# Optimization experiments

Measured on AMD Instinct MI355X. Metric: run time of the kernel, lower is better.

## Reference

```python
import jax, jax.numpy as jnp
import numpy as np

B, S, D, H, E, K = 4, 2048, 1024, 4096, 8, 2
CAP_RATIO = 1.05


def setup_inputs() -> dict:
    key = jax.random.key(0)
    k0, k1, k2, k3 = jax.random.split(key, 4)
    x = jax.random.normal(k0, (B, S, D), jnp.float32)
    # router gating weight (xavier-uniform-ish scale)
    Wg = jax.random.normal(k1, (E, D), jnp.float32) * np.float32(np.sqrt(2.0 / (D + E)))
    W1 = jax.random.normal(k2, (E, D, H), jnp.float32) * np.float32(0.02)
    b1 = jnp.zeros((E, H), jnp.float32)
    W2 = jax.random.normal(k3, (E, H, D), jnp.float32) * np.float32(0.02)
    b2 = jnp.zeros((E, D), jnp.float32)
    return {"x": x, "Wg": Wg, "W1": W1, "b1": b1, "W2": W2, "b2": b2}


def reference(x, Wg, W1, b1, W2, b2):
    Bs, Ss, Dd = x.shape
    T = Bs * Ss
    C = int(round(K * T * CAP_RATIO / E))  # static buffer capacity per expert
    xf = x.reshape(T, Dd)

    # --- router (eval mode: no noise) ---
    logits = xf @ Wg.T                       # (T, E)
    gates = jax.nn.softmax(logits, axis=-1)  # (T, E)
    topv, topi = jax.lax.top_k(gates, K)     # (T, K)

    # --- capacity-limited dispatch: FCFS over slot-major (slot, token) order ---
    idx_sm = topi.T.reshape(-1)                              # (K*T,) slot-major expert ids
    oh = jax.nn.one_hot(idx_sm, E, dtype=jnp.int32)          # (K*T, E)
    pos_sm = (jnp.cumsum(oh, axis=0) * oh).sum(-1) - 1       # 0-based rank within expert
    within_sm = pos_sm < C
    pos_sm = jnp.where(within_sm, pos_sm, C)                 # C == out-of-bounds sentinel
    pos = pos_sm.reshape(K, T).T                             # (T, K)
    within = within_sm.reshape(K, T).T                       # (T, K) bool

    # --- combine weights: mask dropped slots, renormalize over active slots ---
    w = topv * within.astype(topv.dtype)
    sums = w.sum(-1, keepdims=True)
    w = jnp.where(sums > 0, w / sums, w)

    # --- scatter tokens into per-expert capacity buffers ---
    e_flat = topi.reshape(-1)                                # (T*K,)
    pos_flat = pos.reshape(-1)                               # (T*K,)
    x_ts = jnp.broadcast_to(xf[:, None, :], (T, K, Dd)).reshape(T * K, Dd)
    expert_in = jnp.zeros((E, C, Dd), x.dtype).at[e_flat, pos_flat].set(x_ts, mode='drop')

    # --- per-expert MLP (grouped GEMM) ---
    h = jax.nn.gelu(jnp.einsum('ecd,edh->ech', expert_in, W1) + b1[:, None, :], approximate=False)
    o = jnp.einsum('ech,ehd->ecd', h, W2) + b2[:, None, :]   # (E, C, D)

    # --- gather back and weighted combine (dropped slots gather 0) ---
    y_ts = o.at[e_flat, pos_flat].get(mode='fill', fill_value=0).reshape(T, K, Dd)
    y = jnp.einsum('tk,tkd->td', w, y_ts)                    # (T, D)

    # --- auxiliary losses ---
    imp = gates.sum(0)                                       # (E,)
    l_imp = (jnp.std(imp) / (imp.mean() + 1e-6)) ** 2
    tpe = (oh * within_sm[:, None].astype(jnp.int32)).sum(0).astype(jnp.float32)
    l_load = (jnp.std(tpe) / (tpe.mean() + 1e-6)) ** 2
    l_aux = 0.5 * (l_imp + l_load)

    return y.reshape(Bs, Ss, Dd), l_aux, l_load
```

## Files before the change

kernel.cpp:

```cpp
#include <hip/hip_runtime.h>
#include <math.h>

typedef short short8v __attribute__((ext_vector_type(8)));
typedef float f32x4 __attribute__((ext_vector_type(4)));
typedef unsigned short ushort4v __attribute__((ext_vector_type(4)));

#define T_TOK 8192
#define DDIM 1024
#define HDIM 4096
#define NE 8
#define CCAP 2150
#define CPAD 2304

__device__ __forceinline__ unsigned short f2bf(float f) {
  union { float f; unsigned u; } a; a.f = f;
  unsigned r = a.u + 0x7fffu + ((a.u >> 16) & 1u);
  return (unsigned short)(r >> 16);
}
__device__ __forceinline__ float bf2f(unsigned short h) {
  union { unsigned u; float f; } a; a.u = ((unsigned)h) << 16;
  return a.f;
}

__global__ __launch_bounds__(256) void router_kernel(
    const float* __restrict__ x, const float* __restrict__ Wg,
    int2* __restrict__ topi, float2* __restrict__ topv,
    float* __restrict__ blkimp) {
  __shared__ float wg[NE * DDIM];
  __shared__ float gsh[4][NE];
  int tid = threadIdx.x;
  for (int i = tid; i < NE * DDIM / 4; i += 256)
    ((float4*)wg)[i] = ((const float4*)Wg)[i];
  __syncthreads();
  int w = tid >> 6, lane = tid & 63;
  int t = blockIdx.x * 4 + w;
  const float* xr = x + (size_t)t * DDIM;
  float p[NE] = {0.f, 0.f, 0.f, 0.f, 0.f, 0.f, 0.f, 0.f};
#pragma unroll
  for (int j = 0; j < 16; ++j) {
    float xv = xr[lane + 64 * j];
#pragma unroll
    for (int e = 0; e < NE; ++e)
      p[e] = fmaf(xv, wg[e * DDIM + lane + 64 * j], p[e]);
  }
#pragma unroll
  for (int e = 0; e < NE; ++e) {
#pragma unroll
    for (int off = 32; off > 0; off >>= 1) p[e] += __shfl_xor(p[e], off, 64);
  }
  float mx = p[0];
#pragma unroll
  for (int e = 1; e < NE; ++e) mx = fmaxf(mx, p[e]);
  float g[NE];
  float s = 0.f;
#pragma unroll
  for (int e = 0; e < NE; ++e) { g[e] = expf(p[e] - mx); s += g[e]; }
  float inv = 1.0f / s;
#pragma unroll
  for (int e = 0; e < NE; ++e) g[e] *= inv;
  int i0 = 0; float v0 = g[0];
#pragma unroll
  for (int e = 1; e < NE; ++e) if (g[e] > v0) { v0 = g[e]; i0 = e; }
  int i1 = -1; float v1 = -1.0f;
#pragma unroll
  for (int e = 0; e < NE; ++e)
    if (e != i0 && g[e] > v1) { v1 = g[e]; i1 = e; }
  if (lane == 0) {
    topi[t] = make_int2(i0, i1);
    topv[t] = make_float2(v0, v1);
#pragma unroll
    for (int e = 0; e < NE; ++e) gsh[w][e] = g[e];
  }
  __syncthreads();
  if (tid < NE)
    blkimp[blockIdx.x * NE + tid] =
        gsh[0][tid] + gsh[1][tid] + gsh[2][tid] + gsh[3][tid];
}

__global__ __launch_bounds__(256) void dispatch_kernel(
    const int2* __restrict__ topi, const float2* __restrict__ topv,
    const float* __restrict__ blkimp, int2* __restrict__ posmj,
    float2* __restrict__ wmaj, float* __restrict__ tail) {
  __shared__ unsigned char eid[2 * T_TOK];
  __shared__ unsigned short possm[2 * T_TOK];
  __shared__ int cnt_sh[NE];
  __shared__ float part[32][NE];
  int tid = threadIdx.x;
  for (int i = tid; i < T_TOK; i += 256) {
    int2 ti = topi[i];
    eid[i] = (unsigned char)ti.x;
    eid[T_TOK + i] = (unsigned char)ti.y;
  }
  __syncthreads();
  if (tid < 64) {
    int lane = tid;
    unsigned long long low = (1ull << lane) - 1ull;
    int c0 = 0, c1 = 0, c2 = 0, c3 = 0, c4 = 0, c5 = 0, c6 = 0, c7 = 0;
    for (int base = 0; base < 2 * T_TOK; base += 64) {
      int e = eid[base + lane];
      unsigned long long m0 = __ballot(e == 0);
      unsigned long long m1 = __ballot(e == 1);
      unsigned long long m2 = __ballot(e == 2);
      unsigned long long m3 = __ballot(e == 3);
      unsigned long long m4 = __ballot(e == 4);
      unsigned long long m5 = __ballot(e == 5);
      unsigned long long m6 = __ballot(e == 6);
      unsigned long long m7 = __ballot(e == 7);
      int rank = 0;
      if (e == 0) rank = c0 + __popcll(m0 & low);
      if (e == 1) rank = c1 + __popcll(m1 & low);
      if (e == 2) rank = c2 + __popcll(m2 & low);
      if (e == 3) rank = c3 + __popcll(m3 & low);
      if (e == 4) rank = c4 + __popcll(m4 & low);
      if (e == 5) rank = c5 + __popcll(m5 & low);
      if (e == 6) rank = c6 + __popcll(m6 & low);
      if (e == 7) rank = c7 + __popcll(m7 & low);
      possm[base + lane] = (unsigned short)((rank < CCAP) ? rank : CCAP);
      c0 += __popcll(m0); c1 += __popcll(m1); c2 += __popcll(m2);
      c3 += __popcll(m3); c4 += __popcll(m4); c5 += __popcll(m5);
      c6 += __popcll(m6); c7 += __popcll(m7);
    }
    if (lane == 0) {
      cnt_sh[0] = c0; cnt_sh[1] = c1; cnt_sh[2] = c2; cnt_sh[3] = c3;
      cnt_sh[4] = c4; cnt_sh[5] = c5; cnt_sh[6] = c6; cnt_sh[7] = c7;
    }
  }
  __syncthreads();
  for (int t = tid; t < T_TOK; t += 256) {
    int p0 = possm[t], p1 = possm[T_TOK + t];
    float2 tv = topv[t];
    float w0 = (p0 < CCAP) ? tv.x : 0.0f;
    float w1 = (p1 < CCAP) ? tv.y : 0.0f;
    float s = w0 + w1;
    if (s > 0.0f) { w0 /= s; w1 /= s; }
    posmj[t] = make_int2(p0, p1);
    wmaj[t] = make_float2(w0, w1);
  }
  {
    int sl = tid >> 3, e8 = tid & 7;
    float s = 0.f;
    for (int b = sl; b < 2048; b += 32) s += blkimp[b * NE + e8];
    part[sl][e8] = s;
  }
  __syncthreads();
  if (tid == 0) {
    float imp[NE], te[NE];
    for (int e = 0; e < NE; ++e) {
      float s = 0.f;
      for (int j = 0; j < 32; ++j) s += part[j][e];
      imp[e] = s;
      int c = cnt_sh[e];
      te[e] = (float)(c < CCAP ? c : CCAP);
    }
    float mi = 0.f, mt = 0.f;
    for (int e = 0; e < NE; ++e) { mi += imp[e]; mt += te[e]; }
    mi *= 0.125f; mt *= 0.125f;
    float vi = 0.f, vt = 0.f;
    for (int e = 0; e < NE; ++e) {
      vi += (imp[e] - mi) * (imp[e] - mi);
      vt += (te[e] - mt) * (te[e] - mt);
    }
    vi *= 0.125f; vt *= 0.125f;
    float ai = sqrtf(vi) / (mi + 1e-6f);
    float at = sqrtf(vt) / (mt + 1e-6f);
    tail[0] = 0.5f * (ai * ai + at * at);
    tail[1] = at * at;
  }
}

__global__ __launch_bounds__(256) void scatter_kernel(
    const float* __restrict__ x, const int2* __restrict__ topi,
    const int2* __restrict__ posmj, unsigned short* __restrict__ ein) {
  int tid = threadIdx.x;
  int gid = blockIdx.x * 4 + (tid >> 6);
  int lane = tid & 63;
  int t = gid >> 1, k = gid & 1;
  int2 pp = posmj[t];
  int p = k ? pp.y : pp.x;
  if (p >= CCAP) return;
  int2 ii = topi[t];
  int e = k ? ii.y : ii.x;
  const float4* src = (const float4*)(x + (size_t)t * DDIM);
  unsigned short* dst = ein + ((size_t)e * CPAD + p) * DDIM;
#pragma unroll
  for (int j = 0; j < 4; ++j) {
    int c = j * 64 + lane;
    float4 v = src[c];
    ushort4v o;
    o.x = f2bf(v.x); o.y = f2bf(v.y); o.z = f2bf(v.z); o.w = f2bf(v.w);
    *(ushort4v*)(dst + (size_t)c * 4) = o;
  }
}

__global__ __launch_bounds__(256) void transpose_cvt_kernel(
    const float* __restrict__ W, unsigned short* __restrict__ WT, int R,
    int Cc) {
  __shared__ unsigned short tile[64][72];
  int rt = R >> 6, ct = Cc >> 6;
  int per_e = rt * ct;
  int e = blockIdx.x / per_e;
  int rem = blockIdx.x % per_e;
  int tr = rem % rt, tc = rem / rt;
  int r0 = tr << 6, c0 = tc << 6;
  const float* We = W + (size_t)e * R * Cc;
  unsigned short* WTe = WT + (size_t)e * R * Cc;
  int tid = threadIdx.x;
  {
    int rl = tid >> 2, cb = (tid & 3) << 4;
    const float* src = We + (size_t)(r0 + rl) * Cc + c0 + cb;
#pragma unroll
    for (int j = 0; j < 16; j += 4) {
      float4 v = *(const float4*)(src + j);
      tile[rl][cb + j + 0] = f2bf(v.x);
      tile[rl][cb + j + 1] = f2bf(v.y);
      tile[rl][cb + j + 2] = f2bf(v.z);
      tile[rl][cb + j + 3] = f2bf(v.w);
    }
  }
  __syncthreads();
  {
    int cl = tid >> 2, rb = (tid & 3) << 4;
    unsigned short* dst = WTe + (size_t)(c0 + cl) * R + r0 + rb;
#pragma unroll
    for (int j = 0; j < 16; j += 4) {
      ushort4v o;
      o.x = tile[rb + j + 0][cl];
      o.y = tile[rb + j + 1][cl];
      o.z = tile[rb + j + 2][cl];
      o.w = tile[rb + j + 3][cl];
      *(ushort4v*)(dst + j) = o;
    }
  }
}

template <bool GELU>
__global__ __launch_bounds__(512, 2) void gemm256_rs(
    const unsigned short* __restrict__ A, const unsigned short* __restrict__ B,
    const float* __restrict__ bias, unsigned short* __restrict__ Out0,
    unsigned short* __restrict__ Out1, int M, int N, int Kz, int Ksub, int NT,
    int mt, int nt) {
  __shared__ __align__(16) char smem[131072];
  int nwg = gridDim.x;
  int bid = blockIdx.x;
  int swz = (bid & 7) * (nwg >> 3) + (bid >> 3);
  int bm = swz % mt;
  int r = swz / mt;
  int bn = r % nt;
  int r2 = r / nt;
  int e = r2 & 7;
  int ks = r2 >> 3;
  unsigned short* Outp = ks ? Out1 : Out0;
  int koff = ks * Ksub;

  int tid = threadIdx.x;
  int w = tid >> 6, lane = tid & 63;
  int wm = w >> 2, wn = w & 3;
  int fr = lane & 15, g = lane >> 4;
  size_t Kzs = (size_t)Kz;
  const char* Ab = (const char*)(A + ((size_t)e * M + (size_t)bm * 256) * Kzs + koff);
  const char* Bb = (const char*)(B + ((size_t)e * N + (size_t)bn * 256) * Kzs + koff);

  size_t ro0 = (size_t)(w * 16 + fr) * Kzs * 2 + (size_t)g * 16;
  size_t ro1 = ro0 + (size_t)128 * Kzs * 2;
  int ld0 = (w << 10) + lane * 16;
  int ld1 = ((8 + w) << 10) + lane * 16;

  short8v st[8];
  auto gload = [&](const char* a, const char* b) {
    st[0] = *(const short8v*)(a + ro0);
    st[1] = *(const short8v*)(a + ro1);
    st[2] = *(const short8v*)(a + ro0 + 64);
    st[3] = *(const short8v*)(a + ro1 + 64);
    st[4] = *(const short8v*)(b + ro0);
    st[5] = *(const short8v*)(b + ro1);
    st[6] = *(const short8v*)(b + ro0 + 64);
    st[7] = *(const short8v*)(b + ro1 + 64);
  };
  auto swrite = [&](int buf) {
    char* p = smem + (buf << 15);
    *(short8v*)(p + ld0) = st[0];
    *(short8v*)(p + ld1) = st[1];
    *(short8v*)(p + 16384 + ld0) = st[2];
    *(short8v*)(p + 16384 + ld1) = st[3];
    *(short8v*)(p + 65536 + ld0) = st[4];
    *(short8v*)(p + 65536 + ld1) = st[5];
    *(short8v*)(p + 65536 + 16384 + ld0) = st[6];
    *(short8v*)(p + 65536 + 16384 + ld1) = st[7];
  };
  auto lda = [&](int buf, int kk, int m16) -> short8v {
    return *(const short8v*)(smem + (buf << 15) + (kk << 14) + (m16 << 10) +
                             lane * 16);
  };
  auto ldb = [&](int buf, int kk, int n16) -> short8v {
    return *(const short8v*)(smem + 65536 + (buf << 15) + (kk << 14) +
                             (n16 << 10) + lane * 16);
  };

  f32x4 acc[8][4] = {};

  gload(Ab, Bb);
  swrite(0);
  gload(Ab + 128, Bb + 128);
  __syncthreads();

  for (int t = 0; t < NT; ++t) {
    int c = t & 1;
#pragma unroll
    for (int kk = 0; kk < 2; ++kk) {
      short8v bv4[4], av;
#pragma unroll
      for (int n = 0; n < 4; ++n) bv4[n] = ldb(c, kk, wn * 4 + n);
#pragma unroll
      for (int m = 0; m < 8; ++m) {
        av = lda(c, kk, wm * 8 + m);
#pragma unroll
        for (int n = 0; n < 4; ++n)
          acc[m][n] = __builtin_amdgcn_mfma_f32_16x16x32_bf16(av, bv4[n],
                                                              acc[m][n], 0, 0, 0);
      }
    }
    if (t + 1 < NT) swrite(c ^ 1);
    if (t + 2 < NT)
      gload(Ab + (size_t)(t + 2) * 128, Bb + (size_t)(t + 2) * 128);
    __syncthreads();
  }

  float bv[4];
#pragma unroll
  for (int n = 0; n < 4; ++n)
    bv[n] = (ks == 0)
                ? bias[(size_t)e * N + (size_t)bn * 256 + wn * 64 + n * 16 + fr]
                : 0.0f;
  char* wreg = smem + w * 16384;
#pragma unroll
  for (int m = 0; m < 8; ++m)
#pragma unroll
    for (int n = 0; n < 4; ++n)
#pragma unroll
      for (int j = 0; j < 4; ++j) {
        float v = acc[m][n][j] + bv[n];
        if (GELU) v = 0.5f * v * (1.0f + erff(v * 0.70710678118654752f));
        int rl = m * 16 + g * 4 + j;
        *(unsigned short*)(wreg + rl * 128 + (n * 16 + fr) * 2) = f2bf(v);
      }
  unsigned short* Oe = Outp +
                       ((size_t)e * M + (size_t)bm * 256 + (size_t)wm * 128) * N +
                       (size_t)bn * 256 + (size_t)wn * 64;
#pragma unroll
  for (int pass = 0; pass < 16; ++pass) {
    int rr = pass * 8 + (lane >> 3);
    int ch = lane & 7;
    short8v vv = *(const short8v*)(wreg + rr * 128 + ch * 16);
    *(short8v*)(Oe + (size_t)rr * N + ch * 8) = vv;
  }
}

__global__ __launch_bounds__(256) void gather_kernel(
    const unsigned short* __restrict__ obufA,
    const unsigned short* __restrict__ obufB, const int2* __restrict__ topi,
    const int2* __restrict__ posmj, const float2* __restrict__ wmaj,
    float* __restrict__ y) {
  int tid = threadIdx.x;
  int w = tid >> 6, lane = tid & 63;
  int t = blockIdx.x * 4 + w;
  int2 pp = posmj[t];
  int2 ii = topi[t];
  float2 ww = wmaj[t];
  float* yr = y + (size_t)t * DDIM;
  size_t o0 = ((size_t)ii.x * CPAD + pp.x) * DDIM;
  size_t o1 = ((size_t)ii.y * CPAD + pp.y) * DDIM;
  bool v0 = pp.x < CCAP, v1 = pp.y < CCAP;
#pragma unroll
  for (int j = 0; j < 4; ++j) {
    int c = j * 64 + lane;
    float ax = 0.f, ay = 0.f, az = 0.f, aw = 0.f;
    if (v0) {
      ushort4v a = *(const ushort4v*)(obufA + o0 + (size_t)c * 4);
      ushort4v b = *(const ushort4v*)(obufB + o0 + (size_t)c * 4);
      ax += ww.x * (bf2f(a.x) + bf2f(b.x));
      ay += ww.x * (bf2f(a.y) + bf2f(b.y));
      az += ww.x * (bf2f(a.z) + bf2f(b.z));
      aw += ww.x * (bf2f(a.w) + bf2f(b.w));
    }
    if (v1) {
      ushort4v a = *(const ushort4v*)(obufA + o1 + (size_t)c * 4);
      ushort4v b = *(const ushort4v*)(obufB + o1 + (size_t)c * 4);
      ax += ww.y * (bf2f(a.x) + bf2f(b.x));
      ay += ww.y * (bf2f(a.y) + bf2f(b.y));
      az += ww.y * (bf2f(a.z) + bf2f(b.z));
      aw += ww.y * (bf2f(a.w) + bf2f(b.w));
    }
    ((float4*)yr)[c] = make_float4(ax, ay, az, aw);
  }
}

extern "C" void kernel_launch(void* const* d_in, const int* in_sizes, int n_in,
                              void* d_out, int out_size, void* d_ws,
                              size_t ws_size, hipStream_t stream) {
  (void)in_sizes; (void)n_in; (void)out_size; (void)ws_size;
  const float* x = (const float*)d_in[0];
  const float* Wg = (const float*)d_in[1];
  const float* W1 = (const float*)d_in[2];
  const float* b1 = (const float*)d_in[3];
  const float* W2 = (const float*)d_in[4];
  const float* b2 = (const float*)d_in[5];
  float* out = (float*)d_out;

  char* ws = (char*)d_ws;
  size_t off = 0;
  auto alloc = [&](size_t b) {
    char* p = ws + off;
    off += (b + 255) & ~(size_t)255;
    return p;
  };
  unsigned short* ein = (unsigned short*)alloc((size_t)NE * CPAD * DDIM * 2);
  unsigned short* hbuf = (unsigned short*)alloc((size_t)NE * CPAD * HDIM * 2);
  unsigned short* obuf = (unsigned short*)alloc((size_t)NE * CPAD * DDIM * 2);
  unsigned short* w1t = (unsigned short*)alloc((size_t)NE * HDIM * DDIM * 2);
  unsigned short* w2t = (unsigned short*)alloc((size_t)NE * DDIM * HDIM * 2);
  int2* topi = (int2*)alloc(T_TOK * sizeof(int2));
  float2* topv = (float2*)alloc(T_TOK * sizeof(float2));
  int2* posmj = (int2*)alloc(T_TOK * sizeof(int2));
  float2* wmaj = (float2*)alloc(T_TOK * sizeof(float2));
  float* blkimp = (float*)alloc(2048 * NE * sizeof(float));

  transpose_cvt_kernel<<<NE * (DDIM / 64) * (HDIM / 64), 256, 0, stream>>>(
      W1, w1t, DDIM, HDIM);
  transpose_cvt_kernel<<<NE * (HDIM / 64) * (DDIM / 64), 256, 0, stream>>>(
      W2, w2t, HDIM, DDIM);
  router_kernel<<<T_TOK / 4, 256, 0, stream>>>(x, Wg, topi, topv, blkimp);
  dispatch_kernel<<<1, 256, 0, stream>>>(topi, topv, blkimp, posmj, wmaj,
                                         out + (size_t)T_TOK * DDIM);
  scatter_kernel<<<(2 * T_TOK) / 4, 256, 0, stream>>>(x, topi, posmj, ein);

  gemm256_rs<true><<<NE * 9 * 16, 512, 0, stream>>>(
      ein, w1t, b1, hbuf, hbuf, CPAD, HDIM, DDIM, DDIM, DDIM / 64, 9, 16);
  gemm256_rs<false><<<NE * 9 * 4 * 2, 512, 0, stream>>>(
      hbuf, w2t, b2, obuf, ein, CPAD, DDIM, HDIM, HDIM / 2, HDIM / 128, 9, 4);

  gather_kernel<<<T_TOK / 4, 256, 0, stream>>>(obuf, ein, topi, posmj, wmaj,
                                               out);
}
```

Baseline: 665.8 us.

## Load GEMM operands directly from global memory into MFMA registers, dropping LDS staging

The grouped expert GEMMs no longer stage A/B tiles through double-buffered shared memory with barriers. Each wave now loads its MFMA operand fragments straight from global memory, and the K loop count becomes a template parameter so it can be unrolled. The epilogue is also reworked to write out through a small 4KB-per-wave buffer in four chunks, which cuts LDS to 32KB. This removes LDS traffic and block-wide syncs, but each fragment is re-read by several waves through L1/L2. The global loads are strided narrow row reads rather than coalesced tiles, and there is no software prefetch.

```diff
diff --git a/kernel.cpp b/kernel.cpp
--- a/kernel.cpp
+++ b/kernel.cpp
@@ -233,13 +233,13 @@
   }
 }
 
-template <bool GELU>
-__global__ __launch_bounds__(512, 2) void gemm256_rs(
+template <int NT, bool GELU>
+__global__ __launch_bounds__(512) void gemm256_nolds(
     const unsigned short* __restrict__ A, const unsigned short* __restrict__ B,
     const float* __restrict__ bias, unsigned short* __restrict__ Out0,
-    unsigned short* __restrict__ Out1, int M, int N, int Kz, int Ksub, int NT,
-    int mt, int nt) {
-  __shared__ __align__(16) char smem[131072];
+    unsigned short* __restrict__ Out1, int M, int N, int Kz, int Ksub, int mt,
+    int nt) {
+  __shared__ __align__(16) char smem[32768];
   int nwg = gridDim.x;
   int bid = blockIdx.x;
   int swz = (bid & 7) * (nwg >> 3) + (bid >> 3);
@@ -257,72 +257,33 @@
   int wm = w >> 2, wn = w & 3;
   int fr = lane & 15, g = lane >> 4;
   size_t Kzs = (size_t)Kz;
-  const char* Ab = (const char*)(A + ((size_t)e * M + (size_t)bm * 256) * Kzs + koff);
-  const char* Bb = (const char*)(B + ((size_t)e * N + (size_t)bn * 256) * Kzs + koff);
-
-  size_t ro0 = (size_t)(w * 16 + fr) * Kzs * 2 + (size_t)g * 16;
-  size_t ro1 = ro0 + (size_t)128 * Kzs * 2;
-  int ld0 = (w << 10) + lane * 16;
-  int ld1 = ((8 + w) << 10) + lane * 16;
-
-  short8v st[8];
-  auto gload = [&](const char* a, const char* b) {
-    st[0] = *(const short8v*)(a + ro0);
-    st[1] = *(const short8v*)(a + ro1);
-    st[2] = *(const short8v*)(a + ro0 + 64);
-    st[3] = *(const short8v*)(a + ro1 + 64);
-    st[4] = *(const short8v*)(b + ro0);
-    st[5] = *(const short8v*)(b + ro1);
-    st[6] = *(const short8v*)(b + ro0 + 64);
-    st[7] = *(const short8v*)(b + ro1 + 64);
-  };
-  auto swrite = [&](int buf) {
-    char* p = smem + (buf << 15);
-    *(short8v*)(p + ld0) = st[0];
-    *(short8v*)(p + ld1) = st[1];
-    *(short8v*)(p + 16384 + ld0) = st[2];
-    *(short8v*)(p + 16384 + ld1) = st[3];
-    *(short8v*)(p + 65536 + ld0) = st[4];
-    *(short8v*)(p + 65536 + ld1) = st[5];
-    *(short8v*)(p + 65536 + 16384 + ld0) = st[6];
-    *(short8v*)(p + 65536 + 16384 + ld1) = st[7];
-  };
-  auto lda = [&](int buf, int kk, int m16) -> short8v {
-    return *(const short8v*)(smem + (buf << 15) + (kk << 14) + (m16 << 10) +
-                             lane * 16);
-  };
-  auto ldb = [&](int buf, int kk, int n16) -> short8v {
-    return *(const short8v*)(smem + 65536 + (buf << 15) + (kk << 14) +
-                             (n16 << 10) + lane * 16);
-  };
+  const unsigned short* Ap =
+      A + ((size_t)e * M + (size_t)bm * 256 + wm * 128 + fr) * Kzs + koff +
+      g * 8;
+  const unsigned short* Bp =
+      B + ((size_t)e * N + (size_t)bn * 256 + wn * 64 + fr) * Kzs + koff +
+      g * 8;
 
   f32x4 acc[8][4] = {};
 
-  gload(Ab, Bb);
-  swrite(0);
-  gload(Ab + 128, Bb + 128);
-  __syncthreads();
-
+#pragma unroll 4
   for (int t = 0; t < NT; ++t) {
-    int c = t & 1;
 #pragma unroll
     for (int kk = 0; kk < 2; ++kk) {
-      short8v bv4[4], av;
-#pragma unroll
-      for (int n = 0; n < 4; ++n) bv4[n] = ldb(c, kk, wn * 4 + n);
+      int ko = t * 64 + kk * 32;
+      short8v Bv[4];
+#pragma unroll
+      for (int n = 0; n < 4; ++n)
+        Bv[n] = *(const short8v*)(Bp + (size_t)(n * 16) * Kzs + ko);
 #pragma unroll
       for (int m = 0; m < 8; ++m) {
-        av = lda(c, kk, wm * 8 + m);
+        short8v av = *(const short8v*)(Ap + (size_t)(m * 16) * Kzs + ko);
 #pragma unroll
         for (int n = 0; n < 4; ++n)
-          acc[m][n] = __builtin_amdgcn_mfma_f32_16x16x32_bf16(av, bv4[n],
+          acc[m][n] = __builtin_amdgcn_mfma_f32_16x16x32_bf16(av, Bv[n],
                                                               acc[m][n], 0, 0, 0);
       }
     }
-    if (t + 1 < NT) swrite(c ^ 1);
-    if (t + 2 < NT)
-      gload(Ab + (size_t)(t + 2) * 128, Bb + (size_t)(t + 2) * 128);
-    __syncthreads();
   }
 
   float bv[4];
@@ -331,27 +292,29 @@
     bv[n] = (ks == 0)
                 ? bias[(size_t)e * N + (size_t)bn * 256 + wn * 64 + n * 16 + fr]
                 : 0.0f;
-  char* wreg = smem + w * 16384;
-#pragma unroll
-  for (int m = 0; m < 8; ++m)
-#pragma unroll
-    for (int n = 0; n < 4; ++n)
-#pragma unroll
-      for (int j = 0; j < 4; ++j) {
-        float v = acc[m][n][j] + bv[n];
-        if (GELU) v = 0.5f * v * (1.0f + erff(v * 0.70710678118654752f));
-        int rl = m * 16 + g * 4 + j;
-        *(unsigned short*)(wreg + rl * 128 + (n * 16 + fr) * 2) = f2bf(v);
-      }
+  unsigned short* wb = (unsigned short*)(smem + w * 4096);
   unsigned short* Oe = Outp +
                        ((size_t)e * M + (size_t)bm * 256 + (size_t)wm * 128) * N +
                        (size_t)bn * 256 + (size_t)wn * 64;
 #pragma unroll
-  for (int pass = 0; pass < 16; ++pass) {
-    int rr = pass * 8 + (lane >> 3);
-    int ch = lane & 7;
-    short8v vv = *(const short8v*)(wreg + rr * 128 + ch * 16);
-    *(short8v*)(Oe + (size_t)rr * N + ch * 8) = vv;
+  for (int h = 0; h < 4; ++h) {
+#pragma unroll
+    for (int m2 = 0; m2 < 2; ++m2)
+#pragma unroll
+      for (int n = 0; n < 4; ++n)
+#pragma unroll
+        for (int j = 0; j < 4; ++j) {
+          float v = acc[h * 2 + m2][n][j] + bv[n];
+          if (GELU) v = 0.5f * v * (1.0f + erff(v * 0.70710678118654752f));
+          wb[(m2 * 16 + g * 4 + j) * 64 + n * 16 + fr] = f2bf(v);
+        }
+#pragma unroll
+    for (int p = 0; p < 4; ++p) {
+      int rr = p * 8 + (lane >> 3);
+      int ch = lane & 7;
+      short8v vv = *(const short8v*)(wb + rr * 64 + ch * 8);
+      *(short8v*)(Oe + (size_t)(h * 32 + rr) * N + ch * 8) = vv;
+    }
   }
 }
 
@@ -433,10 +396,10 @@
                                          out + (size_t)T_TOK * DDIM);
   scatter_kernel<<<(2 * T_TOK) / 4, 256, 0, stream>>>(x, topi, posmj, ein);
 
-  gemm256_rs<true><<<NE * 9 * 16, 512, 0, stream>>>(
-      ein, w1t, b1, hbuf, hbuf, CPAD, HDIM, DDIM, DDIM, DDIM / 64, 9, 16);
-  gemm256_rs<false><<<NE * 9 * 4 * 2, 512, 0, stream>>>(
-      hbuf, w2t, b2, obuf, ein, CPAD, DDIM, HDIM, HDIM / 2, HDIM / 128, 9, 4);
+  gemm256_nolds<16, true><<<NE * 9 * 16, 512, 0, stream>>>(
+      ein, w1t, b1, hbuf, hbuf, CPAD, HDIM, DDIM, DDIM, 9, 16);
+  gemm256_nolds<32, false><<<NE * 9 * 4 * 2, 512, 0, stream>>>(
+      hbuf, w2t, b2, obuf, ein, CPAD, DDIM, HDIM, HDIM / 2, 9, 4);
 
   gather_kernel<<<T_TOK / 4, 256, 0, stream>>>(obuf, ein, topi, posmj, wmaj,
                                                out);
```

Result: slower. 1.240 ms (+86.3%).

## Split first expert GEMM into 256-tile and 128-tile kernels to balance waves

Applied to the files above, without the earlier changes.

The first grouped GEMM (up-projection with GELU) is split by output column range. The first half of the N tiles stays on the 256x256 kernel, and the second half runs on a new 128x128-tile kernel with 256 threads. A bn0 offset parameter is added so each launch covers its own column range. The aim is to reduce wave quantization and tail imbalance across CUs. In exchange, the smaller tiles have lower arithmetic intensity and the change adds an extra launch.

```diff
diff --git a/kernel.cpp b/kernel.cpp
--- a/kernel.cpp
+++ b/kernel.cpp
@@ -238,14 +238,14 @@
     const unsigned short* __restrict__ A, const unsigned short* __restrict__ B,
     const float* __restrict__ bias, unsigned short* __restrict__ Out0,
     unsigned short* __restrict__ Out1, int M, int N, int Kz, int Ksub, int NT,
-    int mt, int nt) {
+    int mt, int nt, int bn0) {
   __shared__ __align__(16) char smem[131072];
   int nwg = gridDim.x;
   int bid = blockIdx.x;
   int swz = (bid & 7) * (nwg >> 3) + (bid >> 3);
   int bm = swz % mt;
   int r = swz / mt;
-  int bn = r % nt;
+  int bn = r % nt + bn0;
   int r2 = r / nt;
   int e = r2 & 7;
   int ks = r2 >> 3;
@@ -351,6 +351,120 @@
     int rr = pass * 8 + (lane >> 3);
     int ch = lane & 7;
     short8v vv = *(const short8v*)(wreg + rr * 128 + ch * 16);
+    *(short8v*)(Oe + (size_t)rr * N + ch * 8) = vv;
+  }
+}
+
+template <bool GELU>
+__global__ __launch_bounds__(256) void gemm128_rs(
+    const unsigned short* __restrict__ A, const unsigned short* __restrict__ B,
+    const float* __restrict__ bias, unsigned short* __restrict__ Out, int M,
+    int N, int Kz, int NT, int mt, int nt, int bn0) {
+  __shared__ __align__(16) char smem[65536];
+  int nwg = gridDim.x;
+  int bid = blockIdx.x;
+  int swz = (bid & 7) * (nwg >> 3) + (bid >> 3);
+  int bm = swz % mt;
+  int r = swz / mt;
+  int bn = r % nt + bn0;
+  int e = (r / nt) & 7;
+
+  int tid = threadIdx.x;
+  int w = tid >> 6, lane = tid & 63;
+  int wm = w >> 1, wn = w & 1;
+  int fr = lane & 15, g = lane >> 4;
+  size_t Kzs = (size_t)Kz;
+  const char* Ab = (const char*)(A + ((size_t)e * M + (size_t)bm * 128) * Kzs);
+  const char* Bb = (const char*)(B + ((size_t)e * N + (size_t)bn * 128) * Kzs);
+
+  size_t ro0 = (size_t)(w * 16 + fr) * Kzs * 2 + (size_t)g * 16;
+  size_t ro1 = ro0 + (size_t)64 * Kzs * 2;
+  int ld0 = (w << 10) + lane * 16;
+  int ld1 = ((4 + w) << 10) + lane * 16;
+
+  short8v st[8];
+  auto gload = [&](const char* a, const char* b) {
+    st[0] = *(const short8v*)(a + ro0);
+    st[1] = *(const short8v*)(a + ro1);
+    st[2] = *(const short8v*)(a + ro0 + 64);
+    st[3] = *(const short8v*)(a + ro1 + 64);
+    st[4] = *(const short8v*)(b + ro0);
+    st[5] = *(const short8v*)(b + ro1);
+    st[6] = *(const short8v*)(b + ro0 + 64);
+    st[7] = *(const short8v*)(b + ro1 + 64);
+  };
+  auto swrite = [&](int buf) {
+    char* p = smem + (buf << 14);
+    *(short8v*)(p + ld0) = st[0];
+    *(short8v*)(p + ld1) = st[1];
+    *(short8v*)(p + 8192 + ld0) = st[2];
+    *(short8v*)(p + 8192 + ld1) = st[3];
+    *(short8v*)(p + 32768 + ld0) = st[4];
+    *(short8v*)(p + 32768 + ld1) = st[5];
+    *(short8v*)(p + 32768 + 8192 + ld0) = st[6];
+    *(short8v*)(p + 32768 + 8192 + ld1) = st[7];
+  };
+  auto lda = [&](int buf, int kk, int m16) -> short8v {
+    return *(const short8v*)(smem + (buf << 14) + (kk << 13) + (m16 << 10) +
+                             lane * 16);
+  };
+  auto ldb = [&](int buf, int kk, int n16) -> short8v {
+    return *(const short8v*)(smem + 32768 + (buf << 14) + (kk << 13) +
+                             (n16 << 10) + lane * 16);
+  };
+
+  f32x4 acc[4][4] = {};
+
+  gload(Ab, Bb);
+  swrite(0);
+  gload(Ab + 128, Bb + 128);
+  __syncthreads();
+
+  for (int t = 0; t < NT; ++t) {
+    int c = t & 1;
+#pragma unroll
+    for (int kk = 0; kk < 2; ++kk) {
+      short8v bv4[4], av;
+#pragma unroll
+      for (int n = 0; n < 4; ++n) bv4[n] = ldb(c, kk, wn * 4 + n);
+#pragma unroll
+      for (int m = 0; m < 4; ++m) {
+        av = lda(c, kk, wm * 4 + m);
+#pragma unroll
+        for (int n = 0; n < 4; ++n)
+          acc[m][n] = __builtin_amdgcn_mfma_f32_16x16x32_bf16(av, bv4[n],
+                                                              acc[m][n], 0, 0, 0);
+      }
+    }
+    if (t + 1 < NT) swrite(c ^ 1);
+    if (t + 2 < NT)
+      gload(Ab + (size_t)(t + 2) * 128, Bb + (size_t)(t + 2) * 128);
+    __syncthreads();
+  }
+
+  float bv[4];
+#pragma unroll
+  for (int n = 0; n < 4; ++n)
+    bv[n] = bias[(size_t)e * N + (size_t)bn * 128 + wn * 64 + n * 16 + fr];
+  unsigned short* wb = (unsigned short*)(smem + w * 8192);
+#pragma unroll
+  for (int m = 0; m < 4; ++m)
+#pragma unroll
+    for (int n = 0; n < 4; ++n)
+#pragma unroll
+      for (int j = 0; j < 4; ++j) {
+        float v = acc[m][n][j] + bv[n];
+        if (GELU) v = 0.5f * v * (1.0f + erff(v * 0.70710678118654752f));
+        wb[(m * 16 + g * 4 + j) * 64 + n * 16 + fr] = f2bf(v);
+      }
+  unsigned short* Oe = Out + ((size_t)e * M + (size_t)bm * 128 +
+                              (size_t)wm * 64) * (size_t)N +
+                       (size_t)bn * 128 + (size_t)wn * 64;
+#pragma unroll
+  for (int p = 0; p < 8; ++p) {
+    int rr = p * 8 + (lane >> 3);
+    int ch = lane & 7;
+    short8v vv = *(const short8v*)(wb + rr * 64 + ch * 8);
     *(short8v*)(Oe + (size_t)rr * N + ch * 8) = vv;
   }
 }
@@ -433,10 +547,13 @@
                                          out + (size_t)T_TOK * DDIM);
   scatter_kernel<<<(2 * T_TOK) / 4, 256, 0, stream>>>(x, topi, posmj, ein);
 
-  gemm256_rs<true><<<NE * 9 * 16, 512, 0, stream>>>(
-      ein, w1t, b1, hbuf, hbuf, CPAD, HDIM, DDIM, DDIM, DDIM / 64, 9, 16);
+  gemm256_rs<true><<<NE * 9 * 8, 512, 0, stream>>>(
+      ein, w1t, b1, hbuf, hbuf, CPAD, HDIM, DDIM, DDIM, DDIM / 64, 9, 8, 0);
+  gemm128_rs<true><<<NE * 18 * 16, 256, 0, stream>>>(
+      ein, w1t, b1, hbuf, CPAD, HDIM, DDIM, DDIM / 64, 18, 16, 16);
   gemm256_rs<false><<<NE * 9 * 4 * 2, 512, 0, stream>>>(
-      hbuf, w2t, b2, obuf, ein, CPAD, DDIM, HDIM, HDIM / 2, HDIM / 128, 9, 4);
+      hbuf, w2t, b2, obuf, ein, CPAD, DDIM, HDIM, HDIM / 2, HDIM / 128, 9, 4,
+      0);
 
   gather_kernel<<<T_TOK / 4, 256, 0, stream>>>(obuf, ein, topi, posmj, wmaj,
                                                out);
```

New measurement: 747.2 us. 1.12x slower.

## Parallelize dispatch rank scan across four waves with chunked prefix sums

Applied to the files above, without the earlier changes.

The capacity ranking in the dispatch kernel previously ran serially on one wavefront over all 16384 slot entries. It now splits the work into 64 chunks of 256 entries. All four waves count per-expert occurrences in their chunks, one wave builds an exclusive prefix over the chunk counts with shuffles, and all four waves then assign ranks in parallel. This shortens the serial dependency chain in a single-block kernel, at the cost of a second pass over the expert ids and two extra barriers.

```diff
diff --git a/kernel.cpp b/kernel.cpp
--- a/kernel.cpp
+++ b/kernel.cpp
@@ -83,46 +83,87 @@
     float2* __restrict__ wmaj, float* __restrict__ tail) {
   __shared__ unsigned char eid[2 * T_TOK];
   __shared__ unsigned short possm[2 * T_TOK];
+  __shared__ int ccnt[64][NE];
+  __shared__ int cpre[64][NE];
   __shared__ int cnt_sh[NE];
   __shared__ float part[32][NE];
   int tid = threadIdx.x;
+  int w = tid >> 6, lane = tid & 63;
   for (int i = tid; i < T_TOK; i += 256) {
     int2 ti = topi[i];
     eid[i] = (unsigned char)ti.x;
     eid[T_TOK + i] = (unsigned char)ti.y;
   }
   __syncthreads();
+  for (int ch = w; ch < 64; ch += 4) {
+    int c0 = 0, c1 = 0, c2 = 0, c3 = 0, c4 = 0, c5 = 0, c6 = 0, c7 = 0;
+    int base = ch * 256;
+#pragma unroll
+    for (int g2 = 0; g2 < 4; ++g2) {
+      int e = eid[base + g2 * 64 + lane];
+      c0 += __popcll(__ballot(e == 0));
+      c1 += __popcll(__ballot(e == 1));
+      c2 += __popcll(__ballot(e == 2));
+      c3 += __popcll(__ballot(e == 3));
+      c4 += __popcll(__ballot(e == 4));
+      c5 += __popcll(__ballot(e == 5));
+      c6 += __popcll(__ballot(e == 6));
+      c7 += __popcll(__ballot(e == 7));
+    }
+    if (lane == 0) {
+      ccnt[ch][0] = c0; ccnt[ch][1] = c1; ccnt[ch][2] = c2; ccnt[ch][3] = c3;
+      ccnt[ch][4] = c4; ccnt[ch][5] = c5; ccnt[ch][6] = c6; ccnt[ch][7] = c7;
+    }
+  }
+  __syncthreads();
   if (tid < 64) {
-    int lane = tid;
+#pragma unroll
+    for (int e = 0; e < NE; ++e) {
+      int own = ccnt[lane][e];
+      int inc = own;
+#pragma unroll
+      for (int off = 1; off < 64; off <<= 1) {
+        int tv = __shfl_up(inc, off, 64);
+        if (lane >= off) inc += tv;
+      }
+      cpre[lane][e] = inc - own;
+      if (lane == 63) cnt_sh[e] = inc;
+    }
+  }
+  __syncthreads();
+  {
     unsigned long long low = (1ull << lane) - 1ull;
-    int c0 = 0, c1 = 0, c2 = 0, c3 = 0, c4 = 0, c5 = 0, c6 = 0, c7 = 0;
-    for (int base = 0; base < 2 * T_TOK; base += 64) {
-      int e = eid[base + lane];
-      unsigned long long m0 = __ballot(e == 0);
-      unsigned long long m1 = __ballot(e == 1);
-      unsigned long long m2 = __ballot(e == 2);
-      unsigned long long m3 = __ballot(e == 3);
-      unsigned long long m4 = __ballot(e == 4);
-      unsigned long long m5 = __ballot(e == 5);
-      unsigned long long m6 = __ballot(e == 6);
-      unsigned long long m7 = __ballot(e == 7);
-      int rank = 0;
-      if (e == 0) rank = c0 + __popcll(m0 & low);
-      if (e == 1) rank = c1 + __popcll(m1 & low);
-      if (e == 2) rank = c2 + __popcll(m2 & low);
-      if (e == 3) rank = c3 + __popcll(m3 & low);
-      if (e == 4) rank = c4 + __popcll(m4 & low);
-      if (e == 5) rank = c5 + __popcll(m5 & low);
-      if (e == 6) rank = c6 + __popcll(m6 & low);
-      if (e == 7) rank = c7 + __popcll(m7 & low);
-      possm[base + lane] = (unsigned short)((rank < CCAP) ? rank : CCAP);
-      c0 += __popcll(m0); c1 += __popcll(m1); c2 += __popcll(m2);
-      c3 += __popcll(m3); c4 += __popcll(m4); c5 += __popcll(m5);
-      c6 += __popcll(m6); c7 += __popcll(m7);
-    }
-    if (lane == 0) {
-      cnt_sh[0] = c0; cnt_sh[1] = c1; cnt_sh[2] = c2; cnt_sh[3] = c3;
-      cnt_sh[4] = c4; cnt_sh[5] = c5; cnt_sh[6] = c6; cnt_sh[7] = c7;
+    for (int ch = w; ch < 64; ch += 4) {
+      int r0 = cpre[ch][0], r1 = cpre[ch][1], r2 = cpre[ch][2],
+          r3 = cpre[ch][3], r4 = cpre[ch][4], r5 = cpre[ch][5],
+          r6 = cpre[ch][6], r7 = cpre[ch][7];
+      int base = ch * 256;
+#pragma unroll
+      for (int g2 = 0; g2 < 4; ++g2) {
+        int idx = base + g2 * 64 + lane;
+        int e = eid[idx];
+        unsigned long long m0 = __ballot(e == 0);
+        unsigned long long m1 = __ballot(e == 1);
+        unsigned long long m2 = __ballot(e == 2);
+        unsigned long long m3 = __ballot(e == 3);
+        unsigned long long m4 = __ballot(e == 4);
+        unsigned long long m5 = __ballot(e == 5);
+        unsigned long long m6 = __ballot(e == 6);
+        unsigned long long m7 = __ballot(e == 7);
+        int rank = 0;
+        if (e == 0) rank = r0 + __popcll(m0 & low);
+        if (e == 1) rank = r1 + __popcll(m1 & low);
+        if (e == 2) rank = r2 + __popcll(m2 & low);
+        if (e == 3) rank = r3 + __popcll(m3 & low);
+        if (e == 4) rank = r4 + __popcll(m4 & low);
+        if (e == 5) rank = r5 + __popcll(m5 & low);
+        if (e == 6) rank = r6 + __popcll(m6 & low);
+        if (e == 7) rank = r7 + __popcll(m7 & low);
+        possm[idx] = (unsigned short)((rank < CCAP) ? rank : CCAP);
+        r0 += __popcll(m0); r1 += __popcll(m1); r2 += __popcll(m2);
+        r3 += __popcll(m3); r4 += __popcll(m4); r5 += __popcll(m5);
+        r6 += __popcll(m6); r7 += __popcll(m7);
+      }
     }
   }
   __syncthreads();
```

Measured after the change: 639.0 us (median of 3 runs). 4.0% less time.
